# Kernel optimization log

Hardware: AMD Instinct MI355X
Metric: run time of the kernel (lower is better)

## Reference

```python
import jax, jax.numpy as jnp
import numpy as np

DIM, N_HEADS, N_KV, HEAD_DIM = 4096, 32, 8, 128
REPEATS = N_HEADS // N_KV
SCALE = HEAD_DIM ** -0.5


def apply_rope(x, offset=0):
    # x: [b, h, l, hd]; rotation convention matches the torch source:
    # out_even = xe*cos + xo*sin, out_odd = -xe*sin + xo*cos, interleaved back.
    hd = x.shape[-1]
    l = x.shape[2]
    freqs = 1.0 / 10000.0 ** (jnp.arange(0, hd, 2, dtype=jnp.float32) / hd)  # [hd/2]
    t = jnp.arange(l, dtype=jnp.float32) + offset
    ang = t[:, None] * freqs[None, :]                     # [l, hd/2]
    sin, cos = jnp.sin(ang), jnp.cos(ang)
    xe, xo = x[..., 0::2], x[..., 1::2]                   # [b,h,l,hd/2]
    out = jnp.stack([xe * cos + xo * sin, -xe * sin + xo * cos], axis=-1)
    return out.reshape(x.shape)


def setup_inputs() -> dict:
    key = jax.random.key(0)
    ks = jax.random.split(key, 5)
    b, l = 1, 2048
    x = jax.random.normal(ks[0], (b, l, DIM), dtype=jnp.float32)
    # additive causal mask: 0 on/below diagonal, -1e9 above
    neg = jnp.full((l, l), -1e9, dtype=jnp.float32)
    mask = jnp.triu(neg, k=1)
    wq = jax.random.normal(ks[1], (N_HEADS * HEAD_DIM, DIM), dtype=jnp.float32) * 0.02
    wk = jax.random.normal(ks[2], (N_KV * HEAD_DIM, DIM), dtype=jnp.float32) * 0.02
    wv = jax.random.normal(ks[3], (N_KV * HEAD_DIM, DIM), dtype=jnp.float32) * 0.02
    wo = jax.random.normal(ks[4], (DIM, N_HEADS * HEAD_DIM), dtype=jnp.float32) * 0.02
    return {"x": x, "mask": mask, "wq": wq, "wk": wk, "wv": wv, "wo": wo}


def reference(x, mask, wq, wk, wv, wo):
    b, l, d = x.shape
    q = (x @ wq.T).reshape(b, l, N_HEADS, HEAD_DIM).transpose(0, 2, 1, 3)  # [b,H,l,hd]
    k = (x @ wk.T).reshape(b, l, N_KV, HEAD_DIM).transpose(0, 2, 1, 3)     # [b,Hk,l,hd]
    v = (x @ wv.T).reshape(b, l, N_KV, HEAD_DIM).transpose(0, 2, 1, 3)
    # GQA repeat (head = kv_head*repeats + r, same as torch cat+view)
    k = jnp.repeat(k, REPEATS, axis=1)
    v = jnp.repeat(v, REPEATS, axis=1)
    q = apply_rope(q)
    k = apply_rope(k)
    atn = jnp.einsum('bhqd,bhkd->bhqk', q * SCALE, k) + mask
    atn = jax.nn.softmax(atn.astype(jnp.float32), axis=-1).astype(q.dtype)
    out = jnp.einsum('bhqk,bhkd->bhqd', atn, v)
    out = out.transpose(0, 2, 1, 3).reshape(b, l, -1)
    return (out @ wo.T, k, v)
```

## Files before the change

kernel.cpp:

```cpp
#include <hip/hip_runtime.h>
#include <stdint.h>

#define L_SEQ  2048
#define NHEAD  32
#define NKV    8
#define HD     128
#define DIM    4096
#define KVDIM  1024
#define QKVS   6144
#define SCALE  0.08838834764831845f
#define LOG2E  1.4426950408889634f
#define SM_OFF 12.0f

typedef __attribute__((ext_vector_type(8))) short bf16x8;
typedef __attribute__((ext_vector_type(4))) float f32x4;

#define FENCE() asm volatile("" ::: "memory")

__device__ __forceinline__ unsigned short f2bf(float f) {
    unsigned u = __float_as_uint(f);
    u = (u + 0x7FFFu + ((u >> 16) & 1u)) >> 16;
    return (unsigned short)u;
}
__device__ __forceinline__ float bf2f(unsigned short h) {
    return __uint_as_float(((unsigned)h) << 16);
}
__device__ __forceinline__ void gload_lds16(const void* g, void* l) {
    __builtin_amdgcn_global_load_lds(
        (const __attribute__((address_space(1))) unsigned int*)g,
        (__attribute__((address_space(3))) unsigned int*)l, 16, 0, 0);
}

__global__ void cvt_all(const float* __restrict__ x,  const float* __restrict__ wq,
                        const float* __restrict__ wk, const float* __restrict__ wv,
                        unsigned short* __restrict__ xb, unsigned short* __restrict__ wqb,
                        unsigned short* __restrict__ wkvb) {
    const int N_X = L_SEQ * DIM / 4, N_WQ = DIM * DIM / 4, N_WKV = KVDIM * DIM / 4;
    int i = blockIdx.x * blockDim.x + threadIdx.x;
    int stride = gridDim.x * blockDim.x;
    const int total = N_X + N_WQ + 2 * N_WKV;
    for (; i < total; i += stride) {
        const float* src; unsigned short* dst; int j = i;
        if (j < N_X)                { src = x;  dst = xb; }
        else if ((j -= N_X) < N_WQ) { src = wq; dst = wqb; }
        else if ((j -= N_WQ) < N_WKV) { src = wk; dst = wkvb; }
        else { j -= N_WKV; src = wv; dst = wkvb + (size_t)KVDIM * DIM; }
        float4 v = ((const float4*)src)[j];
        ushort4 o;
        o.x = f2bf(v.x); o.y = f2bf(v.y); o.z = f2bf(v.z); o.w = f2bf(v.w);
        ((ushort4*)dst)[j] = o;
    }
}

__global__ void cvt_f32_bf16(const float* __restrict__ in, unsigned short* __restrict__ out, int n4) {
    int i = blockIdx.x * blockDim.x + threadIdx.x;
    int stride = gridDim.x * blockDim.x;
    for (; i < n4; i += stride) {
        float4 v = ((const float4*)in)[i];
        ushort4 o;
        o.x = f2bf(v.x); o.y = f2bf(v.y); o.z = f2bf(v.z); o.w = f2bf(v.w);
        ((ushort4*)out)[i] = o;
    }
}

__global__ void addf32(float* __restrict__ out, const float* __restrict__ p, int n4) {
    int i = blockIdx.x * blockDim.x + threadIdx.x;
    int stride = gridDim.x * blockDim.x;
    for (; i < n4; i += stride) {
        float4 a = ((const float4*)out)[i];
        float4 b = ((const float4*)p)[i];
        a.x += b.x; a.y += b.y; a.z += b.z; a.w += b.w;
        ((float4*)out)[i] = a;
    }
}

__global__ void rope_table(float2* __restrict__ rt) {
    int i = blockIdx.x * blockDim.x + threadIdx.x;
    if (i >= L_SEQ * 64) return;
    int l = i >> 6, f = i & 63;
    float freq = powf(10000.0f, -(float)f / 64.0f);
    float ang  = (float)l * freq;
    rt[i] = make_float2(cosf(ang), sinf(ang));
}

__global__ void rope_apply(unsigned short* __restrict__ X, const float2* __restrict__ rt,
                           int log2H, int strideShorts, float mul) {
    int i = blockIdx.x * blockDim.x + threadIdx.x;
    int f  = i & 63;
    int hh = (i >> 6) & ((1 << log2H) - 1);
    int l  = i >> (6 + log2H);
    if (l >= L_SEQ) return;
    float2 cs = rt[(l << 6) + f];
    size_t base = (size_t)l * strideShorts + (hh << 7);
    float xe = bf2f(X[base + 2 * f]);
    float xo = bf2f(X[base + 2 * f + 1]);
    X[base + 2 * f]     = f2bf((xe * cs.x + xo * cs.y) * mul);
    X[base + 2 * f + 1] = f2bf((-xe * cs.y + xo * cs.x) * mul);
}

__global__ void kv_out(const unsigned short* __restrict__ KVp, float* __restrict__ KO) {
    int i = blockIdx.x * blockDim.x + threadIdx.x;
    if (i >= L_SEQ * KVDIM) return;
    int d  = i & 127;
    int h8 = (i >> 7) & 7;
    int l  = i >> 10;
    float kv = bf2f(KVp[(size_t)l * QKVS + h8 * HD + d]);
#pragma unroll
    for (int r = 0; r < 4; ++r)
        KO[((size_t)(h8 * 4 + r) * L_SEQ + l) * HD + d] = kv;
}

__global__ void vtrans(const unsigned short* __restrict__ KVp, unsigned short* __restrict__ VT,
                       float* __restrict__ VO) {
    __shared__ unsigned short t[32][33];
    int lt = blockIdx.x * 32;
    int h8 = blockIdx.y >> 2;
    int dt = (blockIdx.y & 3) * 32;
    int tx = threadIdx.x & 31, ty = threadIdx.x >> 5;
#pragma unroll
    for (int yy = ty; yy < 32; yy += 8) {
        unsigned short v = KVp[(size_t)(lt + yy) * QKVS + KVDIM + h8 * HD + dt + tx];
        t[yy][tx] = v;
        float vf = bf2f(v);
#pragma unroll
        for (int r = 0; r < 4; ++r)
            VO[((size_t)(h8 * 4 + r) * L_SEQ + lt + yy) * HD + dt + tx] = vf;
    }
    __syncthreads();
#pragma unroll
    for (int yy = ty; yy < 32; yy += 8)
        VT[(size_t)(h8 * HD + dt + yy) * L_SEQ + lt + tx] = t[tx][yy];
}

template <typename OT, int NF>
__global__ __launch_bounds__(512, 2) void gemm_8ph(const unsigned short* __restrict__ A,
                                                   const unsigned short* __restrict__ B,
                                                   OT* __restrict__ C0, OT* __restrict__ C1,
                                                   int N, int K, int klen) {
    __shared__ __align__(16) char L[65536 + 2 * NF * 8192];
    const int tid = threadIdx.x;
    const int w = tid >> 6, lane = tid & 63;
    const int gx = gridDim.x;
    const int nwg = gx * gridDim.y;
    const int orig = blockIdx.y * gx + blockIdx.x;
    const int swz = (orig & 7) * (nwg >> 3) + (orig >> 3);
    const int m0 = (swz / gx) * 256, n0 = (swz % gx) * (NF * 64);
    const int kbase = blockIdx.z * klen;
    OT* __restrict__ C = blockIdx.z ? C1 : C0;
    const int wr = (w >> 2) & 1;
    const int wc = w & 3;
    const int lr = lane & 15, lg = lane >> 4;
    const int NKT = klen >> 6;
    const int swb = (lr & 7) << 4;

    auto stageA = [&](int slot, int u, int kt) {
        int r  = u * 64 + w * 8 + (lane >> 3);
        int cg = (lane & 7) ^ (r & 7);
        gload_lds16(A + (size_t)(m0 + r) * K + kbase + kt * 64 + cg * 8,
                    L + slot * 32768 + (u * 64 + w * 8) * 128);
    };
    auto stageB = [&](int slot, int u, int kt) {
        int r  = u * 64 + w * 8 + (lane >> 3);
        int cg = (lane & 7) ^ (r & 7);
        gload_lds16(B + (size_t)(n0 + r) * K + kbase + kt * 64 + cg * 8,
                    L + 65536 + slot * (NF * 8192) + (u * 64 + w * 8) * 128);
    };

    const f32x4 fz = {0.f, 0.f, 0.f, 0.f};
    f32x4 acc[8][NF];
#pragma unroll
    for (int m = 0; m < 8; ++m)
#pragma unroll
        for (int n = 0; n < NF; ++n) acc[m][n] = fz;

    bf16x8 bfr[NF][2];

#pragma unroll
    for (int u = 0; u < 4; ++u) stageA(0, u, 0);
#pragma unroll
    for (int u = 0; u < NF; ++u) stageB(0, u, 0);
    if (NKT > 1) {
#pragma unroll
        for (int u = 0; u < NF; ++u) stageB(1, u, 1);
    }
    if constexpr (NF == 4) asm volatile("s_waitcnt vmcnt(4)" ::: "memory");
    else                   asm volatile("s_waitcnt vmcnt(3)" ::: "memory");
    __builtin_amdgcn_s_barrier();
    FENCE();

    for (int kt0 = 0; kt0 < NKT; kt0 += 2) {
#pragma unroll
        for (int kp = 0; kp < 2; ++kp) {
            const int kt = kt0 + kp;
            const int s = kp;
            const char* Abase = L + s * 32768;
            const char* Bbase = L + 65536 + s * (NF * 8192);
#pragma unroll
            for (int q = 0; q < 4; ++q) {
                bf16x8 af[2][2];
#pragma unroll
                for (int mm = 0; mm < 2; ++mm)
#pragma unroll
                    for (int kk = 0; kk < 2; ++kk) {
                        int r = wr * 128 + (q * 2 + mm) * 16 + lr;
                        int b = (kk * 64 + lg * 16) ^ swb;
                        af[mm][kk] = *(const bf16x8*)(Abase + r * 128 + b);
                    }
                if (q == 0) {
#pragma unroll
                    for (int n = 0; n < NF; ++n)
#pragma unroll
                        for (int kk = 0; kk < 2; ++kk) {
                            int r = wc * (NF * 16) + n * 16 + lr;
                            int b = (kk * 64 + lg * 16) ^ swb;
                            bfr[n][kk] = *(const bf16x8*)(Bbase + r * 128 + b);
                        }
                }
                if (q == 0 && kt + 1 < NKT) { stageA(s ^ 1, 0, kt + 1); stageA(s ^ 1, 1, kt + 1); }
                if (q == 1 && kt + 1 < NKT) { stageA(s ^ 1, 2, kt + 1); stageA(s ^ 1, 3, kt + 1); }
                if (q == 2 && kt + 2 < NKT) { stageB(s, 0, kt + 2); stageB(s, 1, kt + 2); }
                if (q == 3) {
                    if (kt + 2 < NKT) {
                        stageB(s, 2, kt + 2);
                        if constexpr (NF == 4) {
                            stageB(s, 3, kt + 2);
                            asm volatile("s_waitcnt vmcnt(4)" ::: "memory");
                        } else {
                            asm volatile("s_waitcnt vmcnt(3)" ::: "memory");
                        }
                    } else {
                        asm volatile("s_waitcnt vmcnt(0)" ::: "memory");
                    }
                }
                FENCE();
                __builtin_amdgcn_s_barrier();
                FENCE();
                __builtin_amdgcn_s_setprio(1);
#pragma unroll
                for (int mm = 0; mm < 2; ++mm)
#pragma unroll
                    for (int n = 0; n < NF; ++n)
#pragma unroll
                        for (int kk = 0; kk < 2; ++kk)
                            acc[q * 2 + mm][n] = __builtin_amdgcn_mfma_f32_16x16x32_bf16(
                                af[mm][kk], bfr[n][kk], acc[q * 2 + mm][n], 0, 0, 0);
                __builtin_amdgcn_s_setprio(0);
                FENCE();
                __builtin_amdgcn_s_barrier();
                FENCE();
            }
        }
    }
#pragma unroll
    for (int m = 0; m < 8; ++m) {
        int mrow = m0 + wr * 128 + m * 16 + lg * 4;
#pragma unroll
        for (int n = 0; n < NF; ++n) {
            int ncol = n0 + wc * (NF * 16) + n * 16 + lr;
#pragma unroll
            for (int r = 0; r < 4; ++r) {
                float v = acc[m][n][r];
                if constexpr (sizeof(OT) == 2) C[(size_t)(mrow + r) * N + ncol] = f2bf(v);
                else                           C[(size_t)(mrow + r) * N + ncol] = v;
            }
        }
    }
}

__global__ __launch_bounds__(256, 4) void attn_fwd(const unsigned short* __restrict__ Q,
                                                   const unsigned short* __restrict__ KVp,
                                                   const unsigned short* __restrict__ VT,
                                                   unsigned short* __restrict__ AO) {
    __shared__ __align__(16) unsigned short Ks[64 * 128];
    __shared__ __align__(16) unsigned short Vs[128 * 64];
    __shared__ __align__(16) unsigned short P[4][16][64];
    const int tid = threadIdx.x, w = tid >> 6, lane = tid & 63;
    const int idx = blockIdx.x;
    const int h8  = idx & 7;
    const int h   = (h8 << 2) + ((idx >> 3) & 3);
    const int u   = idx >> 5;
    const int t   = u & 7, quart = u >> 3;
    const int qb  = (quart == 0) ? 31 - t : (quart == 1) ? 16 + t
                  : (quart == 2) ? 15 - t : t;
    const int lr = lane & 15, lg = lane >> 4;
    const int r0 = qb * 64 + w * 16;

    bf16x8 qf[4];
    {
        const unsigned short* qrow = Q + (size_t)(r0 + lr) * QKVS + h * HD + lg * 8;
#pragma unroll
        for (int kd = 0; kd < 4; ++kd) qf[kd] = *(const bf16x8*)(qrow + kd * 32);
    }

    bf16x8 ones;
#pragma unroll
    for (int z = 0; z < 8; ++z) ones[z] = (short)0x3F80;

    const f32x4 fz = {0.f, 0.f, 0.f, 0.f};
    f32x4 o[9];
#pragma unroll
    for (int nd = 0; nd < 9; ++nd) o[nd] = fz;

    const int nkv = qb + 1;
    for (int kv = 0; kv < nkv; ++kv) {
        const int kv0 = kv * 64;
#pragma unroll
        for (int c = 0; c < 4; ++c) {
            int krow = w * 16 + c * 4 + (lane >> 4);
            int kcg  = (lane & 15) ^ (krow & 7);
            gload_lds16(KVp + (size_t)(kv0 + krow) * QKVS + h8 * HD + kcg * 8,
                        Ks + (w * 16 + c * 4) * 128);
            int vrow = w * 32 + c * 8 + (lane >> 3);
            int vcg  = (lane & 7) ^ (vrow & 7);
            gload_lds16(VT + (size_t)(h8 * HD + vrow) * L_SEQ + kv0 + vcg * 8,
                        Vs + (w * 32 + c * 8) * 64);
        }
        __syncthreads();
        f32x4 s[4];
#pragma unroll
        for (int ni = 0; ni < 4; ++ni) s[ni] = fz;
        __builtin_amdgcn_s_setprio(1);
#pragma unroll
        for (int ni = 0; ni < 4; ++ni) {
            bf16x8 kf[4];
#pragma unroll
            for (int kd = 0; kd < 4; ++kd)
                kf[kd] = *(const bf16x8*)(Ks + (ni * 16 + lr) * 128 +
                                          (((kd * 4 + lg) ^ (lr & 7)) * 8));
#pragma unroll
            for (int kd = 0; kd < 4; ++kd)
                s[ni] = __builtin_amdgcn_mfma_f32_16x16x32_bf16(qf[kd], kf[kd], s[ni], 0, 0, 0);
        }
        __builtin_amdgcn_s_setprio(0);
        {
            const bool need_mask = (kv0 + 63) > r0;
#pragma unroll
            for (int ni = 0; ni < 4; ++ni)
#pragma unroll
                for (int rr = 0; rr < 4; ++rr) {
                    float p = __builtin_amdgcn_exp2f(s[ni][rr] - SM_OFF);
                    if (need_mask) {
                        int col = kv0 + ni * 16 + lr;
                        int row = r0 + lg * 4 + rr;
                        p = (col > row) ? 0.f : p;
                    }
                    s[ni][rr] = p;
                }
            char* Pb = (char*)&P[w][0][0];
#pragma unroll
            for (int ni = 0; ni < 4; ni += 2)
#pragma unroll
                for (int rr = 0; rr < 4; ++rr) {
                    unsigned pk;
                    asm("v_cvt_pk_bf16_f32 %0, %1, %2" : "=v"(pk) : "v"(s[ni][rr]), "v"(s[ni + 1][rr]));
                    const int row = lg * 4 + rr;
                    const int sw = (row & 7) << 4;
                    *(unsigned short*)(Pb + ((row * 128 + (ni * 16 + lr) * 2) ^ sw)) = (unsigned short)pk;
                    *(unsigned short*)(Pb + ((row * 128 + ((ni + 1) * 16 + lr) * 2) ^ sw)) =
                        (unsigned short)(pk >> 16);
                }
        }
        bf16x8 pa[2];
        {
            const char* Pb = (const char*)&P[w][0][0];
            const int swr = (lr & 7) << 4;
#pragma unroll
            for (int ks = 0; ks < 2; ++ks)
                pa[ks] = *(const bf16x8*)(Pb + ((lr * 128 + ks * 64 + lg * 16) ^ swr));
        }
        __builtin_amdgcn_s_setprio(1);
#pragma unroll
        for (int nd = 0; nd < 8; ++nd) {
            bf16x8 vf[2];
#pragma unroll
            for (int ks = 0; ks < 2; ++ks)
                vf[ks] = *(const bf16x8*)(Vs + (nd * 16 + lr) * 64 +
                                          (((ks * 4 + lg) ^ (lr & 7)) * 8));
#pragma unroll
            for (int ks = 0; ks < 2; ++ks)
                o[nd] = __builtin_amdgcn_mfma_f32_16x16x32_bf16(pa[ks], vf[ks], o[nd], 0, 0, 0);
        }
#pragma unroll
        for (int ks = 0; ks < 2; ++ks)
            o[8] = __builtin_amdgcn_mfma_f32_16x16x32_bf16(pa[ks], ones, o[8], 0, 0, 0);
        __builtin_amdgcn_s_setprio(0);
        __syncthreads();
    }
    {
        float inv[4];
#pragma unroll
        for (int rr = 0; rr < 4; ++rr) inv[rr] = 1.0f / o[8][rr];
#pragma unroll
        for (int nd = 0; nd < 8; ++nd)
#pragma unroll
            for (int rr = 0; rr < 4; ++rr) {
                int row = r0 + lg * 4 + rr;
                AO[(size_t)row * DIM + h * HD + nd * 16 + lr] = f2bf(o[nd][rr] * inv[rr]);
            }
    }
}

extern "C" void kernel_launch(void* const* d_in, const int* in_sizes, int n_in,
                              void* d_out, int out_size, void* d_ws, size_t ws_size,
                              hipStream_t stream) {
    (void)in_sizes; (void)n_in; (void)out_size; (void)ws_size;
    const float* x  = (const float*)d_in[0];
    const float* wq = (const float*)d_in[2];
    const float* wk = (const float*)d_in[3];
    const float* wv = (const float*)d_in[4];
    const float* wo = (const float*)d_in[5];

    float* out = (float*)d_out;
    float* KO  = out + (size_t)L_SEQ * DIM;
    float* VO  = KO + (size_t)NHEAD * L_SEQ * HD;

    char* ws = (char*)d_ws;
    const size_t MB = 1024 * 1024;
    unsigned short* xb   = (unsigned short*)(ws);
    unsigned short* wqb  = (unsigned short*)(ws + 16 * MB);
    unsigned short* wkvb = (unsigned short*)(ws + 48 * MB);
    unsigned short* qkvp = (unsigned short*)(ws + 64 * MB);
    unsigned short* vtb  = (unsigned short*)(ws + 88 * MB);
    float2*         rt   = (float2*)(ws + 92 * MB);
    unsigned short* aob  = xb;
    unsigned short* wob  = wqb;
    unsigned short* kvp  = qkvp + KVDIM * 4;
    float*          pko  = (float*)(ws + 48 * MB);

    cvt_all<<<2048, 256, 0, stream>>>(x, wq, wk, wv, xb, wqb, wkvb);
    rope_table<<<(L_SEQ * 64) / 256, 256, 0, stream>>>(rt);

    gemm_8ph<unsigned short, 3><<<dim3(QKVS / 192, L_SEQ / 256, 1), 512, 0, stream>>>(
        xb, wqb, qkvp, qkvp, QKVS, DIM, DIM);
    cvt_f32_bf16<<<2048, 256, 0, stream>>>(wo, wob, DIM * DIM / 4);

    rope_apply<<<(L_SEQ * NHEAD * 64) / 256, 256, 0, stream>>>(qkvp, rt, 5, QKVS, SCALE * LOG2E);
    rope_apply<<<(L_SEQ * NKV * 64) / 256, 256, 0, stream>>>(kvp, rt, 3, QKVS, 1.0f);

    kv_out<<<(L_SEQ * KVDIM) / 256, 256, 0, stream>>>(kvp, KO);
    vtrans<<<dim3(L_SEQ / 32, 32), 256, 0, stream>>>(kvp, vtb, VO);

    attn_fwd<<<1024, 256, 0, stream>>>(qkvp, kvp, vtb, aob);

    gemm_8ph<float, 4><<<dim3(DIM / 256, L_SEQ / 256, 2), 512, 0, stream>>>(
        aob, wob, out, pko, DIM, DIM, DIM / 2);
    addf32<<<2048, 256, 0, stream>>>(out, pko, L_SEQ * DIM / 4);
}
```

Measured before the change: 325.0 us.

## Shrink GEMM tiles to 128-row and drop split-K with its reduction kernel

Replaces the 256-row, 8-phase GEMM with a 128-row, 2-phase variant that uses half the LDS and targets 4 workgroups per CU. The output projection no longer splits K across two z-slices plus a separate add kernel; it uses 128x128 tiles over the full K. This removes the partial-sum round trip through memory and one kernel launch, and raises the number of workgroups. The cost is less data reuse per tile and more B traffic per flop.

```diff
diff --git a/kernel.cpp b/kernel.cpp
--- a/kernel.cpp
+++ b/kernel.cpp
@@ -63,17 +63,6 @@
     }
 }
 
-__global__ void addf32(float* __restrict__ out, const float* __restrict__ p, int n4) {
-    int i = blockIdx.x * blockDim.x + threadIdx.x;
-    int stride = gridDim.x * blockDim.x;
-    for (; i < n4; i += stride) {
-        float4 a = ((const float4*)out)[i];
-        float4 b = ((const float4*)p)[i];
-        a.x += b.x; a.y += b.y; a.z += b.z; a.w += b.w;
-        ((float4*)out)[i] = a;
-    }
-}
-
 __global__ void rope_table(float2* __restrict__ rt) {
     int i = blockIdx.x * blockDim.x + threadIdx.x;
     if (i >= L_SEQ * 64) return;
@@ -133,58 +122,54 @@
 }
 
 template <typename OT, int NF>
-__global__ __launch_bounds__(512, 2) void gemm_8ph(const unsigned short* __restrict__ A,
+__global__ __launch_bounds__(512, 4) void gemm_2ph(const unsigned short* __restrict__ A,
                                                    const unsigned short* __restrict__ B,
-                                                   OT* __restrict__ C0, OT* __restrict__ C1,
-                                                   int N, int K, int klen) {
-    __shared__ __align__(16) char L[65536 + 2 * NF * 8192];
+                                                   OT* __restrict__ C, int N, int K) {
+    __shared__ __align__(16) char L[32768 + 2 * NF * 8192];
     const int tid = threadIdx.x;
     const int w = tid >> 6, lane = tid & 63;
     const int gx = gridDim.x;
     const int nwg = gx * gridDim.y;
     const int orig = blockIdx.y * gx + blockIdx.x;
     const int swz = (orig & 7) * (nwg >> 3) + (orig >> 3);
-    const int m0 = (swz / gx) * 256, n0 = (swz % gx) * (NF * 64);
-    const int kbase = blockIdx.z * klen;
-    OT* __restrict__ C = blockIdx.z ? C1 : C0;
+    const int m0 = (swz / gx) * 128, n0 = (swz % gx) * (NF * 64);
     const int wr = (w >> 2) & 1;
     const int wc = w & 3;
     const int lr = lane & 15, lg = lane >> 4;
-    const int NKT = klen >> 6;
+    const int NKT = K >> 6;
     const int swb = (lr & 7) << 4;
 
     auto stageA = [&](int slot, int u, int kt) {
         int r  = u * 64 + w * 8 + (lane >> 3);
         int cg = (lane & 7) ^ (r & 7);
-        gload_lds16(A + (size_t)(m0 + r) * K + kbase + kt * 64 + cg * 8,
-                    L + slot * 32768 + (u * 64 + w * 8) * 128);
+        gload_lds16(A + (size_t)(m0 + r) * K + kt * 64 + cg * 8,
+                    L + slot * 16384 + (u * 64 + w * 8) * 128);
     };
     auto stageB = [&](int slot, int u, int kt) {
         int r  = u * 64 + w * 8 + (lane >> 3);
         int cg = (lane & 7) ^ (r & 7);
-        gload_lds16(B + (size_t)(n0 + r) * K + kbase + kt * 64 + cg * 8,
-                    L + 65536 + slot * (NF * 8192) + (u * 64 + w * 8) * 128);
+        gload_lds16(B + (size_t)(n0 + r) * K + kt * 64 + cg * 8,
+                    L + 32768 + slot * (NF * 8192) + (u * 64 + w * 8) * 128);
     };
 
     const f32x4 fz = {0.f, 0.f, 0.f, 0.f};
-    f32x4 acc[8][NF];
-#pragma unroll
-    for (int m = 0; m < 8; ++m)
+    f32x4 acc[4][NF];
+#pragma unroll
+    for (int m = 0; m < 4; ++m)
 #pragma unroll
         for (int n = 0; n < NF; ++n) acc[m][n] = fz;
 
     bf16x8 bfr[NF][2];
 
-#pragma unroll
-    for (int u = 0; u < 4; ++u) stageA(0, u, 0);
+    stageA(0, 0, 0); stageA(0, 1, 0);
 #pragma unroll
     for (int u = 0; u < NF; ++u) stageB(0, u, 0);
     if (NKT > 1) {
 #pragma unroll
         for (int u = 0; u < NF; ++u) stageB(1, u, 1);
     }
-    if constexpr (NF == 4) asm volatile("s_waitcnt vmcnt(4)" ::: "memory");
-    else                   asm volatile("s_waitcnt vmcnt(3)" ::: "memory");
+    if constexpr (NF == 3) asm volatile("s_waitcnt vmcnt(3)" ::: "memory");
+    else                   asm volatile("s_waitcnt vmcnt(2)" ::: "memory");
     __builtin_amdgcn_s_barrier();
     FENCE();
 
@@ -193,16 +178,16 @@
         for (int kp = 0; kp < 2; ++kp) {
             const int kt = kt0 + kp;
             const int s = kp;
-            const char* Abase = L + s * 32768;
-            const char* Bbase = L + 65536 + s * (NF * 8192);
-#pragma unroll
-            for (int q = 0; q < 4; ++q) {
+            const char* Abase = L + s * 16384;
+            const char* Bbase = L + 32768 + s * (NF * 8192);
+#pragma unroll
+            for (int q = 0; q < 2; ++q) {
                 bf16x8 af[2][2];
 #pragma unroll
                 for (int mm = 0; mm < 2; ++mm)
 #pragma unroll
                     for (int kk = 0; kk < 2; ++kk) {
-                        int r = wr * 128 + (q * 2 + mm) * 16 + lr;
+                        int r = wr * 64 + (q * 2 + mm) * 16 + lr;
                         int b = (kk * 64 + lg * 16) ^ swb;
                         af[mm][kk] = *(const bf16x8*)(Abase + r * 128 + b);
                     }
@@ -217,17 +202,12 @@
                         }
                 }
                 if (q == 0 && kt + 1 < NKT) { stageA(s ^ 1, 0, kt + 1); stageA(s ^ 1, 1, kt + 1); }
-                if (q == 1 && kt + 1 < NKT) { stageA(s ^ 1, 2, kt + 1); stageA(s ^ 1, 3, kt + 1); }
-                if (q == 2 && kt + 2 < NKT) { stageB(s, 0, kt + 2); stageB(s, 1, kt + 2); }
-                if (q == 3) {
+                if (q == 1) {
                     if (kt + 2 < NKT) {
-                        stageB(s, 2, kt + 2);
-                        if constexpr (NF == 4) {
-                            stageB(s, 3, kt + 2);
-                            asm volatile("s_waitcnt vmcnt(4)" ::: "memory");
-                        } else {
-                            asm volatile("s_waitcnt vmcnt(3)" ::: "memory");
-                        }
+#pragma unroll
+                        for (int u = 0; u < NF; ++u) stageB(s, u, kt + 2);
+                        if constexpr (NF == 3) asm volatile("s_waitcnt vmcnt(3)" ::: "memory");
+                        else                   asm volatile("s_waitcnt vmcnt(2)" ::: "memory");
                     } else {
                         asm volatile("s_waitcnt vmcnt(0)" ::: "memory");
                     }
@@ -252,8 +232,8 @@
         }
     }
 #pragma unroll
-    for (int m = 0; m < 8; ++m) {
-        int mrow = m0 + wr * 128 + m * 16 + lg * 4;
+    for (int m = 0; m < 4; ++m) {
+        int mrow = m0 + wr * 64 + m * 16 + lg * 4;
 #pragma unroll
         for (int n = 0; n < NF; ++n) {
             int ncol = n0 + wc * (NF * 16) + n * 16 + lr;
@@ -425,13 +405,12 @@
     unsigned short* aob  = xb;
     unsigned short* wob  = wqb;
     unsigned short* kvp  = qkvp + KVDIM * 4;
-    float*          pko  = (float*)(ws + 48 * MB);
 
     cvt_all<<<2048, 256, 0, stream>>>(x, wq, wk, wv, xb, wqb, wkvb);
     rope_table<<<(L_SEQ * 64) / 256, 256, 0, stream>>>(rt);
 
-    gemm_8ph<unsigned short, 3><<<dim3(QKVS / 192, L_SEQ / 256, 1), 512, 0, stream>>>(
-        xb, wqb, qkvp, qkvp, QKVS, DIM, DIM);
+    gemm_2ph<unsigned short, 3><<<dim3(QKVS / 192, L_SEQ / 128), 512, 0, stream>>>(
+        xb, wqb, qkvp, QKVS, DIM);
     cvt_f32_bf16<<<2048, 256, 0, stream>>>(wo, wob, DIM * DIM / 4);
 
     rope_apply<<<(L_SEQ * NHEAD * 64) / 256, 256, 0, stream>>>(qkvp, rt, 5, QKVS, SCALE * LOG2E);
@@ -442,7 +421,6 @@
 
     attn_fwd<<<1024, 256, 0, stream>>>(qkvp, kvp, vtb, aob);
 
-    gemm_8ph<float, 4><<<dim3(DIM / 256, L_SEQ / 256, 2), 512, 0, stream>>>(
-        aob, wob, out, pko, DIM, DIM, DIM / 2);
-    addf32<<<2048, 256, 0, stream>>>(out, pko, L_SEQ * DIM / 4);
-}
+    gemm_2ph<float, 2><<<dim3(DIM / 128, L_SEQ / 128), 512, 0, stream>>>(
+        aob, wob, out, DIM, DIM);
+}
```

After: 340.4 us. +4.7%, slower.
